# Kernel tuning notes

Hardware: AMD Instinct MI355X
Metric: run time of the kernel (lower is better)

## Reference

```python
import jax, jax.numpy as jnp
import numpy as np
import math

B, S, D, H, L, V = 16, 512, 1024, 16, 128, 32000
DH = D // H


def _posenc(s, d):
    pos = np.arange(s, dtype=np.float32)[:, None]
    div = np.exp(np.arange(0, d, 2, dtype=np.float32) * (-math.log(10000.0) / d))
    pe = np.zeros((s, d), dtype=np.float32)
    pe[:, 0::2] = np.sin(pos * div)
    pe[:, 1::2] = np.cos(pos * div)
    return jnp.asarray(pe)


def _ln(x, g, b):
    m = jnp.mean(x, axis=-1, keepdims=True)
    v = jnp.mean((x - m) ** 2, axis=-1, keepdims=True)
    return (x - m) / jnp.sqrt(v + 1e-5) * g + b


def setup_inputs():
    key = jax.random.key(0)
    ks = jax.random.split(key, 16)
    w = lambda k, *sh: 0.02 * jax.random.normal(k, sh, dtype=jnp.float32)
    return {
        'x': jax.random.randint(ks[0], (B, S), 0, V),
        'embed': w(ks[1], V, D),
        'Wq': w(ks[2], D, D), 'bq': jnp.zeros((D,), jnp.float32),
        'Wk': w(ks[3], D, D), 'bk': jnp.zeros((D,), jnp.float32),
        'Wv': w(ks[4], D, D), 'bv': jnp.zeros((D,), jnp.float32),
        'Wo': w(ks[5], D, D), 'bo': jnp.zeros((D,), jnp.float32),
        'g1': jnp.ones((D,), jnp.float32), 'be1': jnp.zeros((D,), jnp.float32),
        'W1': w(ks[6], D, D), 'bf1': jnp.zeros((D,), jnp.float32),
        'W2': w(ks[7], D, D), 'bf2': jnp.zeros((D,), jnp.float32),
        'g2': jnp.ones((D,), jnp.float32), 'be2': jnp.zeros((D,), jnp.float32),
        'g3': jnp.ones((D,), jnp.float32), 'be3': jnp.zeros((D,), jnp.float32),
        'Wmu': w(ks[8], D, L), 'bmu': jnp.zeros((L,), jnp.float32),
        'Wsig': w(ks[9], D, L), 'bsig': jnp.zeros((L,), jnp.float32),
        'eps': jax.random.normal(ks[10], (B, S, L), dtype=jnp.float32),
    }


def reference(x, embed, Wq, bq, Wk, bk, Wv, bv, Wo, bo, g1, be1, W1, bf1, W2, bf2,
              g2, be2, g3, be3, Wmu, bmu, Wsig, bsig, eps):
    h = embed[x] * jnp.asarray(D ** 0.5, jnp.float32)          # [B,S,D]
    h = h + _posenc(S, D)                                       # dropout = identity (eval)
    h = _ln(h, g1, be1)
    # attention (faithful to source: raw reshape head-split, scale = dh/2)
    Q = (h @ Wq + bq).reshape(B, H, S, DH)
    K = (h @ Wk + bk).reshape(B, H, S, DH)
    Vv = (h @ Wv + bv).reshape(B, H, S, DH)
    scores = jnp.einsum('bhqd,bhkd->bhqk', Q, K) / (DH / 2.0)
    attn = jax.nn.softmax(scores, axis=-1)
    ctx = jnp.einsum('bhqk,bhkd->bhqd', attn, Vv).reshape(B, S, D)
    ctx = ctx @ Wo + bo
    h = h + ctx
    h = _ln(h, g2, be2)
    f = jax.nn.leaky_relu(h @ W1 + bf1, 0.01) @ W2 + bf2
    h = f + f                                                    # source: x = ffn(x); x = x + drop2(x)
    h = _ln(h, g3, be3)
    mu = h @ Wmu + bmu
    sigma = jnp.exp(h @ Wsig + bsig)
    z = mu + sigma * eps
    return z
```

## Files before the change

### kernel.cpp

```cpp
#include <hip/hip_runtime.h>
#include <cstdint>


typedef __bf16 bf16;
typedef __bf16 bf16x8 __attribute__((ext_vector_type(8)));
typedef __bf16 bf16x4 __attribute__((ext_vector_type(4)));
typedef float f32x4 __attribute__((ext_vector_type(4)));

#define MFMA16(a, b, c) __builtin_amdgcn_mfma_f32_16x16x32_bf16((a), (b), (c), 0, 0, 0)

#if __has_builtin(__builtin_amdgcn_exp2f)
#define EXP2F(x) __builtin_amdgcn_exp2f(x)
#else
#define EXP2F(x) exp2f(x)
#endif

__device__ __forceinline__ void async16(const bf16* g, bf16* l) {
  __builtin_amdgcn_global_load_lds(
      (const __attribute__((address_space(1))) unsigned int*)g,
      (__attribute__((address_space(3))) unsigned int*)l, 16, 0, 0);
}

#define VMWAIT(N)                                        \
  do {                                                   \
    asm volatile("s_waitcnt vmcnt(" #N ")" ::: "memory"); \
    __builtin_amdgcn_sched_barrier(0);                   \
  } while (0)
#define BAR() __builtin_amdgcn_s_barrier()

__global__ __launch_bounds__(256) void zero_coefs_kernel(float* __restrict__ p) {
  p[blockIdx.x * 256 + threadIdx.x] = 0.f;
}

struct TP8 {
  const float* src[8];
  const float* gsrc[8];
  bf16* dst[8];
  int ncol[8];
};
__global__ __launch_bounds__(256) void transpose8_kernel(TP8 p) {
  const int z = blockIdx.z;
  const int N = p.ncol[z];
  const int tk = blockIdx.x * 64, tn = blockIdx.y * 64;
  if (tn >= N) return;
  const float* __restrict__ W = p.src[z];
  bf16* __restrict__ Wt = p.dst[z];
  __shared__ float tile[64][65];
  const int a = threadIdx.x >> 6, b = threadIdx.x & 63;
#pragma unroll
  for (int i = 0; i < 16; ++i) {
    int k = a + i * 4;
    tile[k][b] = W[(size_t)(tk + k) * N + tn + b];
  }
  __syncthreads();
  const float* gsc = p.gsrc[z];
  const float gv = gsc ? gsc[tk + b] : 1.0f;
#pragma unroll
  for (int i = 0; i < 16; ++i) {
    int n = a + i * 4;
    Wt[(size_t)(tn + n) * 1024 + tk + b] = (bf16)(tile[b][n] * gv);
  }
}

struct LC3 {
  const float* W[3];
  const float* g[3];
  const float* be[3];
  float* c1[3];
  float* c2[3];
  int N[3];
};
__global__ __launch_bounds__(256) void lncoef_kernel(LC3 p) {
  const int e = blockIdx.y;
  const int N = p.N[e];
  const int n0 = blockIdx.x * 64;
  if (n0 >= N) return;
  const int k0 = blockIdx.z * 64;
  const int w = threadIdx.x >> 6, lane = threadIdx.x & 63;
  const int n = n0 + lane;
  const float* __restrict__ W = p.W[e];
  const float* __restrict__ g = p.g[e];
  const float* __restrict__ be = p.be[e];
  float a1 = 0.f, a2 = 0.f;
#pragma unroll
  for (int i = 0; i < 16; ++i) {
    const int k = k0 + w * 16 + i;
    const float v = W[(size_t)k * N + n];
    a1 += g[k] * v;
    a2 += be[k] * v;
  }
  __shared__ float s1[4][64], s2[4][64];
  s1[w][lane] = a1;
  s2[w][lane] = a2;
  __syncthreads();
  if (w == 0) {
    a1 = s1[0][lane] + s1[1][lane] + s1[2][lane] + s1[3][lane];
    a2 = s2[0][lane] + s2[1][lane] + s2[2][lane] + s2[3][lane];
    atomicAdd(&p.c1[e][n], a1);
    atomicAdd(&p.c2[e][n], a2);
  }
}

__global__ __launch_bounds__(256) void embed_ln_kernel(const int* __restrict__ x,
                                                       const float* __restrict__ emb,
                                                       const float* __restrict__ g,
                                                       const float* __restrict__ be,
                                                       bf16* __restrict__ obf) {
  const int w = threadIdx.x >> 6, lane = threadIdx.x & 63;
  const int row = blockIdx.x * 4 + w;
  const int s = row & 511;
  const int t = x[row];
  const int c0 = lane * 16;
  const float* er = emb + (size_t)t * 1024 + c0;
  float o[16];
#pragma unroll
  for (int i = 0; i < 4; ++i) {
    const float4 e = *(const float4*)(er + i * 4);
    o[i * 4 + 0] = e.x; o[i * 4 + 1] = e.y; o[i * 4 + 2] = e.z; o[i * 4 + 3] = e.w;
  }
#pragma unroll
  for (int p = 0; p < 8; ++p) {
    const int cc = c0 + 2 * p;
    const float freq = __expf((float)cc * (-9.210340371976184f / 1024.0f));
    const float ang = (float)s * freq;
    o[2 * p] = o[2 * p] * 32.0f + __sinf(ang);
    o[2 * p + 1] = o[2 * p + 1] * 32.0f + __cosf(ang);
  }
  float sm = 0.f, q = 0.f;
#pragma unroll
  for (int j = 0; j < 16; ++j) { sm += o[j]; q += o[j] * o[j]; }
#pragma unroll
  for (int off = 1; off < 64; off <<= 1) {
    sm += __shfl_xor(sm, off);
    q += __shfl_xor(q, off);
  }
  const float mean = sm * (1.0f / 1024.0f);
  const float var = q * (1.0f / 1024.0f) - mean * mean;
  const float rstd = rsqrtf(var + 1e-5f);
  bf16 ob[16];
#pragma unroll
  for (int i = 0; i < 4; ++i) {
    const float4 gv = *(const float4*)(g + c0 + i * 4);
    const float4 bv = *(const float4*)(be + c0 + i * 4);
    const float gvv[4] = {gv.x, gv.y, gv.z, gv.w};
    const float bvv[4] = {bv.x, bv.y, bv.z, bv.w};
#pragma unroll
    for (int j = 0; j < 4; ++j)
      ob[i * 4 + j] = (bf16)((o[i * 4 + j] - mean) * rstd * gvv[j] + bvv[j]);
  }
  bf16* dst = obf + (size_t)row * 1024 + c0;
  *(uint4*)dst = *(const uint4*)&ob[0];
  *(uint4*)(dst + 8) = *(const uint4*)&ob[8];
}

__global__ __launch_bounds__(256) void rowstats_kernel(const bf16* __restrict__ in,
                                                       float* __restrict__ rs,
                                                       float* __restrict__ rm) {
  const int w = threadIdx.x >> 6, lane = threadIdx.x & 63;
  const int row = blockIdx.x * 4 + w;
  const int c0 = lane * 16;
  const bf16* src = in + (size_t)row * 1024 + c0;
  const bf16x8 v0 = *(const bf16x8*)src;
  const bf16x8 v1 = *(const bf16x8*)(src + 8);
  float s = 0.f, q = 0.f;
#pragma unroll
  for (int j = 0; j < 8; ++j) {
    const float a = (float)v0[j], b = (float)v1[j];
    s += a + b;
    q += a * a + b * b;
  }
#pragma unroll
  for (int off = 1; off < 64; off <<= 1) {
    s += __shfl_xor(s, off);
    q += __shfl_xor(q, off);
  }
  const float mean = s * (1.0f / 1024.0f);
  const float var = q * (1.0f / 1024.0f) - mean * mean;
  const float rstd = rsqrtf(var + 1e-5f);
  if (lane == 0) {
    rs[row] = rstd;
    rm[row] = -rstd * mean;
  }
}

__device__ __forceinline__ void ld_frags2(const bf16* sm, int rbase, int l15,
                                          int quad, bf16x8 out[2][2]) {
#pragma unroll
  for (int f = 0; f < 2; ++f) {
    const int row = rbase + f * 16 + l15;
    const int rx = row & 7;
#pragma unroll
    for (int h = 0; h < 2; ++h) {
      const int c = (h * 4 + quad) ^ rx;
      out[f][h] = *(const bf16x8*)(sm + (row * 8 + c) * 8);
    }
  }
}

template <int MQ, int NQ>
__device__ __forceinline__ void mma8(const bf16x8 aF[2][2], const bf16x8 bF[2][2],
                                     f32x4 acc[4][4]) {
  __builtin_amdgcn_s_setprio(1);
#pragma unroll
  for (int h = 0; h < 2; ++h)
#pragma unroll
    for (int m2 = 0; m2 < 2; ++m2)
#pragma unroll
      for (int n2 = 0; n2 < 2; ++n2)
        acc[MQ * 2 + m2][NQ * 2 + n2] =
            MFMA16(aF[m2][h], bF[n2][h], acc[MQ * 2 + m2][NQ * 2 + n2]);
  __builtin_amdgcn_s_setprio(0);
}

template <int MODE>
__global__ __launch_bounds__(512, 2) void gemm8_kernel(
    const bf16* __restrict__ A, const bf16* __restrict__ Bt,
    const float* __restrict__ b0f, const float* __restrict__ b1f,
    const float* __restrict__ b2f,
    bf16* __restrict__ o0, bf16* __restrict__ o1, bf16* __restrict__ o2,
    const bf16* __restrict__ residb,
    const float* __restrict__ rsP, const float* __restrict__ rmP,
    int M, int N, int K) {
  (void)M;
  __shared__ __attribute__((aligned(16))) bf16 Asm[2][128 * 64];
  __shared__ __attribute__((aligned(16))) bf16 Bsm[2][256 * 64];
  const int tid = threadIdx.x;
  const int wv = tid >> 6, lane = tid & 63;
  const int quad = lane >> 4, l15 = lane & 15;
  const int wm = wv & 1, wn = wv >> 1;
  const int m0 = blockIdx.x * 128, n0 = blockIdx.y * 256;

  f32x4 acc[4][4];
#pragma unroll
  for (int i = 0; i < 4; ++i)
#pragma unroll
    for (int j = 0; j < 4; ++j) acc[i][j] = {0.f, 0.f, 0.f, 0.f};

  size_t aoff[2], boff[2];
  int slds[2];
#pragma unroll
  for (int i = 0; i < 2; ++i) {
    const int s = tid + i * 512;
    const int r = s >> 3, c = (s & 7) ^ (r & 7);
    aoff[i] = (size_t)(m0 + r) * K + c * 8;
    boff[i] = (size_t)(n0 + r) * K + c * 8;
    slds[i] = s * 8;
  }
  auto stageA = [&](int buf, int t) {
#pragma unroll
    for (int i = 0; i < 2; ++i) async16(A + aoff[i] + t * 64, &Asm[buf][slds[i]]);
  };
  auto stageB = [&](int buf, int hh, int t) {
    const size_t ho = (size_t)hh * 128 * K;
    const int hl = hh * 8192;
#pragma unroll
    for (int i = 0; i < 2; ++i)
      async16(Bt + boff[i] + ho + t * 64, &Bsm[buf][hl + slds[i]]);
  };

  stageB(0, 0, 0); stageB(0, 1, 0); stageA(0, 0);
  stageB(1, 0, 1); stageB(1, 1, 1); stageA(1, 1);
  VMWAIT(6);
  BAR();

  bf16x8 aF[2][2], bF0[2][2], bF1[2][2];
  const int am0 = wm * 64, bn0 = wn * 64;

  auto phases = [&](int ne, int no, bool hn) {
    ld_frags2(&Asm[0][0], am0, l15, quad, aF);
    ld_frags2(&Bsm[0][0], bn0, l15, quad, bF0);
    BAR();
    mma8<0, 0>(aF, bF0, acc);
    BAR();
    ld_frags2(&Bsm[0][0], bn0 + 32, l15, quad, bF1);
    BAR();
    mma8<0, 1>(aF, bF1, acc);
    BAR();
    ld_frags2(&Asm[0][0], am0 + 32, l15, quad, aF);
    if (hn) stageB(0, 0, ne);
    BAR();
    mma8<1, 1>(aF, bF1, acc);
    BAR();
    if (hn) stageB(0, 1, ne);
    BAR();
    mma8<1, 0>(aF, bF0, acc);
    if (hn) { VMWAIT(4); } else { VMWAIT(0); }
    BAR();
    ld_frags2(&Asm[1][0], am0, l15, quad, aF);
    ld_frags2(&Bsm[1][0], bn0, l15, quad, bF0);
    if (hn) stageA(0, ne);
    BAR();
    mma8<0, 0>(aF, bF0, acc);
    BAR();
    ld_frags2(&Bsm[1][0], bn0 + 32, l15, quad, bF1);
    BAR();
    mma8<0, 1>(aF, bF1, acc);
    BAR();
    ld_frags2(&Asm[1][0], am0 + 32, l15, quad, aF);
    if (hn) stageB(1, 0, no);
    BAR();
    mma8<1, 1>(aF, bF1, acc);
    BAR();
    if (hn) { stageB(1, 1, no); stageA(1, no); }
    BAR();
    mma8<1, 0>(aF, bF0, acc);
    if (hn) { VMWAIT(6); }
    BAR();
  };

  const int nIter = K >> 7;
  for (int it = 0; it + 1 < nIter; ++it) phases(2 * it + 2, 2 * it + 3, true);
  phases(0, 0, false);

  const int part = (MODE == 6) ? ((int)blockIdx.y >> 2) : 0;
  bf16* ob = o0;
  const float* bp = b0f;
  if constexpr (MODE == 6) {
    ob = (part == 0) ? o0 : (part == 1 ? o1 : o2);
    bp = (part == 0) ? b0f : (part == 1 ? b1f : b2f);
  }
#pragma unroll
  for (int ni = 0; ni < 4; ++ni) {
    const int col = n0 + wn * 64 + ni * 16 + l15;
    const int cl = (MODE == 6) ? (col - part * 1024) : col;
    const float bv = bp[cl];
    float c1v = 0.f, c2v = 0.f;
    if constexpr (MODE == 4) { c1v = b1f[col]; c2v = b2f[col]; }
#pragma unroll
    for (int mi = 0; mi < 4; ++mi) {
#pragma unroll
      for (int r = 0; r < 4; ++r) {
        const int row = m0 + wm * 64 + mi * 16 + quad * 4 + r;
        const float a = acc[mi][ni][r];
        if constexpr (MODE == 1) {
          const size_t idx = (size_t)row * N + col;
          o0[idx] = (bf16)(a + bv + (float)residb[idx]);
        } else if constexpr (MODE == 4) {
          const float v = rsP[row] * a + rmP[row] * c1v + c2v + bv;
          o0[(size_t)row * N + col] = (bf16)(v > 0.f ? v : 0.01f * v);
        } else if constexpr (MODE == 3) {
          o0[(size_t)row * N + col] = (bf16)(2.0f * (a + bv));
        } else {
          ob[(size_t)row * 1024 + cl] = (bf16)(a + bv);
        }
      }
    }
  }
}

__global__ __launch_bounds__(256) void gemm_musig_z(
    const bf16* __restrict__ A, const bf16* __restrict__ Bt,
    const float* __restrict__ rsP, const float* __restrict__ rmP,
    const float* __restrict__ c1, const float* __restrict__ c2,
    const float* __restrict__ bmu, const float* __restrict__ bsig,
    const float* __restrict__ eps, float* __restrict__ z) {
  __shared__ __attribute__((aligned(16))) bf16 Asm[2][32 * 64];
  __shared__ __attribute__((aligned(16))) bf16 Bsm[2][256 * 64];
  const int tid = threadIdx.x;
  const int wv = tid >> 6, lane = tid & 63;
  const int quad = lane >> 4, l15 = lane & 15;
  const int m0 = blockIdx.x * 32;

  f32x4 acc[2][4];
#pragma unroll
  for (int i = 0; i < 2; ++i)
#pragma unroll
    for (int j = 0; j < 4; ++j) acc[i][j] = {0.f, 0.f, 0.f, 0.f};

  const bf16* Ag;
  int as_;
  {
    const int s = tid;
    const int r = s >> 3, c = (s & 7) ^ (r & 7);
    Ag = A + (size_t)(m0 + r) * 1024 + c * 8;
    as_ = s * 8;
  }
  const bf16* Bg[8];
  int bs_[8];
#pragma unroll
  for (int i = 0; i < 8; ++i) {
    const int s = tid + i * 256;
    const int r = s >> 3, c = (s & 7) ^ (r & 7);
    Bg[i] = Bt + (size_t)r * 1024 + c * 8;
    bs_[i] = s * 8;
  }

  async16(Ag, &Asm[0][as_]);
#pragma unroll
  for (int i = 0; i < 8; ++i) async16(Bg[i], &Bsm[0][bs_[i]]);
  __syncthreads();

  for (int k = 0; k < 16; ++k) {
    const int cur = k & 1, nxt = cur ^ 1;
    bf16x8 af[2][2], bfr[4][2];
#pragma unroll
    for (int mi = 0; mi < 2; ++mi) {
      const int row = mi * 16 + l15;
#pragma unroll
      for (int h = 0; h < 2; ++h) {
        const int pos = (h * 4 + quad) ^ (row & 7);
        af[mi][h] = *(const bf16x8*)(&Asm[cur][(row * 8 + pos) * 8]);
      }
    }
#pragma unroll
    for (int ni = 0; ni < 4; ++ni) {
      const int nr = (ni < 2 ? wv * 32 + ni * 16 : 128 + wv * 32 + (ni - 2) * 16) + l15;
#pragma unroll
      for (int h = 0; h < 2; ++h) {
        const int pos = (h * 4 + quad) ^ (nr & 7);
        bfr[ni][h] = *(const bf16x8*)(&Bsm[cur][(nr * 8 + pos) * 8]);
      }
    }
    if (k + 1 < 16) {
      const int ko = (k + 1) * 64;
      async16(Ag + ko, &Asm[nxt][as_]);
#pragma unroll
      for (int i = 0; i < 8; ++i) async16(Bg[i] + ko, &Bsm[nxt][bs_[i]]);
    }
#pragma unroll
    for (int h = 0; h < 2; ++h)
#pragma unroll
      for (int mi = 0; mi < 2; ++mi)
#pragma unroll
        for (int ni = 0; ni < 4; ++ni)
          acc[mi][ni] = MFMA16(af[mi][h], bfr[ni][h], acc[mi][ni]);
    __syncthreads();
  }

#pragma unroll
  for (int mi = 0; mi < 2; ++mi) {
#pragma unroll
    for (int r = 0; r < 4; ++r) {
      const int row = m0 + mi * 16 + quad * 4 + r;
      const float rs = rsP[row], rm = rmP[row];
#pragma unroll
      for (int cg = 0; cg < 2; ++cg) {
        const int cmu = wv * 32 + cg * 16 + l15;
        const int csg = 128 + cmu;
        const float mu = rs * acc[mi][cg][r] + rm * c1[cmu] + c2[cmu] + bmu[cmu];
        const float sg = rs * acc[mi][2 + cg][r] + rm * c1[csg] + c2[csg] + bsig[cmu];
        z[(size_t)row * 128 + cmu] = mu + __expf(sg) * eps[(size_t)row * 128 + cmu];
      }
    }
  }
}

__global__ __launch_bounds__(256) void vtrans_kernel(const bf16* __restrict__ Vb,
                                                     bf16* __restrict__ VtG) {
  __shared__ float t[64][65];
  const int bh = blockIdx.x, kt = blockIdx.y;
  const int tid = threadIdx.x;
  const bf16* src = Vb + (size_t)bh * 32768 + (size_t)kt * 4096;
#pragma unroll
  for (int i = 0; i < 2; ++i) {
    int s = i * 256 + tid;
    int r = s >> 3, c = (s & 7) * 8;
    bf16x8 v = *(const bf16x8*)(src + (size_t)s * 8);
#pragma unroll
    for (int j = 0; j < 8; ++j) t[r][c + j] = (float)v[j];
  }
  __syncthreads();
  bf16* dst = VtG + (size_t)bh * 32768 + kt * 64;
#pragma unroll
  for (int i = 0; i < 2; ++i) {
    int s = i * 256 + tid;
    int d = s >> 3, kc = (s & 7) * 8;
    bf16 tmp[8];
#pragma unroll
    for (int j = 0; j < 8; ++j) tmp[j] = (bf16)t[kc + j][d];
    *(uint4*)(dst + (size_t)d * 512 + kc) = *(const uint4*)tmp;
  }
}

__global__ __launch_bounds__(256) void attn_kernel(const bf16* __restrict__ Qg,
                                                   const bf16* __restrict__ Kg,
                                                   const bf16* __restrict__ Vt,
                                                   bf16* __restrict__ ctx) {
  __shared__ __attribute__((aligned(16))) bf16 Ksm[128 * 64];
  __shared__ __attribute__((aligned(16))) bf16 Vsm[64 * 128];
  __shared__ __attribute__((aligned(16))) bf16 Psm[4][16 * 128];
  const int tid = threadIdx.x;
  const int w = tid >> 6, lane = tid & 63;
  const int quad = lane >> 4, l15 = lane & 15;
  const int bh = blockIdx.x;
  const size_t base = (size_t)bh * 32768;
  const bf16* Vth = Vt + base;
  const int qbase = blockIdx.y * 128 + w * 32;
  const f32x4 fz = {0.f, 0.f, 0.f, 0.f};

  bf16x8 a[2][2];
#pragma unroll
  for (int qt = 0; qt < 2; ++qt)
#pragma unroll
    for (int hf = 0; hf < 2; ++hf) {
      bf16x8 tq = *(const bf16x8*)(Qg + base +
                   (size_t)(qbase + qt * 16 + l15) * 64 + hf * 32 + quad * 8);
#pragma unroll
      for (int e = 0; e < 8; ++e) tq[e] = (bf16)((float)tq[e] * 0.045111758f);
      a[qt][hf] = tq;
    }

  f32x4 o[2][4];
  float l_i[2][4];
#pragma unroll
  for (int qt = 0; qt < 2; ++qt)
#pragma unroll
    for (int i = 0; i < 4; ++i) { o[qt][i] = fz; l_i[qt][i] = 0.f; }

  for (int kv0 = 0; kv0 < 512; kv0 += 128) {
#pragma unroll
    for (int i = 0; i < 4; ++i) {
      int s = i * 256 + tid;
      int r = s >> 3, c = (s & 7) ^ (r & 7);
      async16(Kg + base + (size_t)(kv0 + r) * 64 + c * 8, &Ksm[s * 8]);
    }
#pragma unroll
    for (int i = 0; i < 4; ++i) {
      int s = i * 256 + tid;
      int d = s >> 4, cs = s & 15;
      int c = (cs & 8) | ((cs & 7) ^ (d & 7));
      async16(Vth + (size_t)d * 512 + kv0 + c * 8, &Vsm[s * 8]);
    }
    __syncthreads();

    f32x4 sc[2][8];
#pragma unroll
    for (int j = 0; j < 8; ++j) {
      const int n = j * 16 + l15;
      const bf16x8 k0 = *(const bf16x8*)(&Ksm[(n * 8 + (quad ^ (n & 7))) * 8]);
      const bf16x8 k1 = *(const bf16x8*)(&Ksm[(n * 8 + ((4 + quad) ^ (n & 7))) * 8]);
      sc[0][j] = MFMA16(a[0][0], k0, fz);
      sc[0][j] = MFMA16(a[0][1], k1, sc[0][j]);
      sc[1][j] = MFMA16(a[1][0], k0, fz);
      sc[1][j] = MFMA16(a[1][1], k1, sc[1][j]);
    }

    bf16* ps = &Psm[w][0];
#pragma unroll
    for (int qt = 0; qt < 2; ++qt) {
#pragma unroll
      for (int r = 0; r < 4; ++r) {
        const int prow = quad * 4 + r;
        float sum = 0.f;
#pragma unroll
        for (int j = 0; j < 8; ++j) {
          const float p = EXP2F(sc[qt][j][r]);
          sum += p;
          const int col = j * 16 + l15;
          const int cc = col >> 3;
          const int ccs = (cc & 8) | ((cc & 7) ^ (prow & 7));
          ps[prow * 128 + ccs * 8 + (col & 7)] = (bf16)p;
        }
        l_i[qt][r] += sum;
      }
#pragma unroll
      for (int c32 = 0; c32 < 4; ++c32) {
        const int pc = c32 * 4 + quad;
        const int pcs = (pc & 8) | ((pc & 7) ^ (l15 & 7));
        const bf16x8 pf = *(const bf16x8*)(ps + l15 * 128 + pcs * 8);
#pragma unroll
        for (int ni = 0; ni < 4; ++ni) {
          const int d = ni * 16 + l15;
          const int vcs = (pc & 8) | ((pc & 7) ^ (d & 7));
          const bf16x8 vf = *(const bf16x8*)(&Vsm[(d * 16 + vcs) * 8]);
          o[qt][ni] = MFMA16(pf, vf, o[qt][ni]);
        }
      }
    }
    __syncthreads();
  }

#pragma unroll
  for (int qt = 0; qt < 2; ++qt) {
#pragma unroll
    for (int r = 0; r < 4; ++r) {
      float l = l_i[qt][r];
      l += __shfl_xor(l, 1);
      l += __shfl_xor(l, 2);
      l += __shfl_xor(l, 4);
      l += __shfl_xor(l, 8);
      const float inv = 1.0f / l;
#pragma unroll
      for (int ni = 0; ni < 4; ++ni)
        ctx[base + (size_t)(qbase + qt * 16 + quad * 4 + r) * 64 + ni * 16 + l15]
            = (bf16)(o[qt][ni][r] * inv);
    }
  }
}

extern "C" void kernel_launch(void* const* d_in, const int* in_sizes, int n_in,
                              void* d_out, int out_size, void* d_ws, size_t ws_size,
                              hipStream_t stream) {
  (void)in_sizes; (void)n_in; (void)out_size; (void)ws_size;
  const int* x = (const int*)d_in[0];
  const float* emb = (const float*)d_in[1];
  const float* Wq = (const float*)d_in[2];
  const float* bq = (const float*)d_in[3];
  const float* Wk = (const float*)d_in[4];
  const float* bkb = (const float*)d_in[5];
  const float* Wv = (const float*)d_in[6];
  const float* bv = (const float*)d_in[7];
  const float* Wo = (const float*)d_in[8];
  const float* bo = (const float*)d_in[9];
  const float* g1 = (const float*)d_in[10];
  const float* be1 = (const float*)d_in[11];
  const float* W1 = (const float*)d_in[12];
  const float* bf1 = (const float*)d_in[13];
  const float* W2 = (const float*)d_in[14];
  const float* bf2 = (const float*)d_in[15];
  const float* g2 = (const float*)d_in[16];
  const float* be2 = (const float*)d_in[17];
  const float* g3 = (const float*)d_in[18];
  const float* be3 = (const float*)d_in[19];
  const float* Wmu = (const float*)d_in[20];
  const float* bmu = (const float*)d_in[21];
  const float* Wsig = (const float*)d_in[22];
  const float* bsig = (const float*)d_in[23];
  const float* eps = (const float*)d_in[24];
  float* z = (float*)d_out;

  const int M = 8192, D = 1024;
  char* ws = (char*)d_ws;
  size_t off = 0;
  auto alloc = [&](size_t b) {
    char* p = ws + off;
    off += (b + 255) & ~(size_t)255;
    return p;
  };
  bf16* wqkvT = (bf16*)alloc((size_t)3072 * 1024 * 2);
  bf16* woT = (bf16*)alloc((size_t)1024 * 1024 * 2);
  bf16* w1T = (bf16*)alloc((size_t)1024 * 1024 * 2);
  bf16* w2T = (bf16*)alloc((size_t)1024 * 1024 * 2);
  bf16* wmsT = (bf16*)alloc((size_t)256 * 1024 * 2);
  bf16* hb = (bf16*)alloc((size_t)M * D * 2);
  bf16* Qb = (bf16*)alloc((size_t)M * D * 2);
  bf16* Kb = (bf16*)alloc((size_t)M * D * 2);
  bf16* Vb = (bf16*)alloc((size_t)M * D * 2);
  bf16* VtG = (bf16*)alloc((size_t)M * D * 2);
  bf16* Cb = (bf16*)alloc((size_t)M * D * 2);
  bf16* h2b = (bf16*)alloc((size_t)M * D * 2);
  bf16* hidb = (bf16*)alloc((size_t)M * D * 2);
  bf16* h4b = (bf16*)alloc((size_t)M * D * 2);
  float* rs2 = (float*)alloc((size_t)M * 4);
  float* rm2 = (float*)alloc((size_t)M * 4);
  float* rs3 = (float*)alloc((size_t)M * 4);
  float* rm3 = (float*)alloc((size_t)M * 4);
  float* coefs = (float*)alloc((size_t)2560 * 4);
  float* c1w1 = coefs;
  float* c2w1 = coefs + 1024;
  float* c1ms = coefs + 2048;
  float* c2ms = coefs + 2304;

  dim3 b256(256);
  dim3 b512(512);

  zero_coefs_kernel<<<10, b256, 0, stream>>>(coefs);

  TP8 tp;
  for (int i = 0; i < 8; ++i) tp.gsrc[i] = nullptr;
  tp.src[0] = Wq;   tp.dst[0] = wqkvT;                        tp.ncol[0] = 1024;
  tp.src[1] = Wk;   tp.dst[1] = wqkvT + (size_t)1024 * 1024;  tp.ncol[1] = 1024;
  tp.src[2] = Wv;   tp.dst[2] = wqkvT + (size_t)2048 * 1024;  tp.ncol[2] = 1024;
  tp.src[3] = Wo;   tp.dst[3] = woT;                          tp.ncol[3] = 1024;
  tp.src[4] = W1;   tp.dst[4] = w1T;   tp.ncol[4] = 1024;     tp.gsrc[4] = g2;
  tp.src[5] = W2;   tp.dst[5] = w2T;                          tp.ncol[5] = 1024;
  tp.src[6] = Wmu;  tp.dst[6] = wmsT;  tp.ncol[6] = 128;      tp.gsrc[6] = g3;
  tp.src[7] = Wsig; tp.dst[7] = wmsT + (size_t)128 * 1024;    tp.ncol[7] = 128;
  tp.gsrc[7] = g3;
  transpose8_kernel<<<dim3(16, 16, 8), b256, 0, stream>>>(tp);

  LC3 lc;
  lc.W[0] = W1;   lc.g[0] = g2; lc.be[0] = be2; lc.c1[0] = c1w1;       lc.c2[0] = c2w1;       lc.N[0] = 1024;
  lc.W[1] = Wmu;  lc.g[1] = g3; lc.be[1] = be3; lc.c1[1] = c1ms;       lc.c2[1] = c2ms;       lc.N[1] = 128;
  lc.W[2] = Wsig; lc.g[2] = g3; lc.be[2] = be3; lc.c1[2] = c1ms + 128; lc.c2[2] = c2ms + 128; lc.N[2] = 128;
  lncoef_kernel<<<dim3(16, 3, 16), b256, 0, stream>>>(lc);

  embed_ln_kernel<<<2048, b256, 0, stream>>>(x, emb, g1, be1, hb);

  gemm8_kernel<6><<<dim3(64, 12), b512, 0, stream>>>(hb, wqkvT, bq, bkb, bv,
                                                     Qb, Kb, Vb, nullptr,
                                                     nullptr, nullptr, M, 3072, D);
  vtrans_kernel<<<dim3(256, 8), b256, 0, stream>>>(Vb, VtG);
  attn_kernel<<<dim3(256, 4), b256, 0, stream>>>(Qb, Kb, VtG, Cb);

  gemm8_kernel<1><<<dim3(64, 4), b512, 0, stream>>>(Cb, woT, bo, nullptr, nullptr,
                                                    h2b, nullptr, nullptr, hb,
                                                    nullptr, nullptr, M, D, D);
  rowstats_kernel<<<2048, b256, 0, stream>>>(h2b, rs2, rm2);
  gemm8_kernel<4><<<dim3(64, 4), b512, 0, stream>>>(h2b, w1T, bf1, c1w1, c2w1,
                                                    hidb, nullptr, nullptr, nullptr,
                                                    rs2, rm2, M, D, D);
  gemm8_kernel<3><<<dim3(64, 4), b512, 0, stream>>>(hidb, w2T, bf2, nullptr, nullptr,
                                                    h4b, nullptr, nullptr, nullptr,
                                                    nullptr, nullptr, M, D, D);
  rowstats_kernel<<<2048, b256, 0, stream>>>(h4b, rs3, rm3);
  gemm_musig_z<<<dim3(256), b256, 0, stream>>>(h4b, wmsT, rs3, rm3, c1ms, c2ms,
                                               bmu, bsig, eps, z);
}
```

Measured before the change: 431.6 us.

## Fuse LayerNorm row statistics into GEMM epilogues and LN coefficients into transpose

The two rowstats kernels are removed. Instead, the Wo and W2 GEMM epilogues accumulate per-row sum and sum-of-squares of their fp32 outputs using shuffles and atomics, and the consumers compute mean and rstd from those sums. The lncoef kernel is folded into the weight-transpose kernel, which reuses its shared-memory tile to build the gamma/beta projection coefficients. This removes three launches and two full re-reads of the activations. In exchange it adds global atomics per row segment and a larger zeroing pass, and the statistics now come from unrounded fp32 values instead of the bf16-stored outputs.

```diff
diff --git a/kernel.cpp b/kernel.cpp
--- a/kernel.cpp
+++ b/kernel.cpp
@@ -35,7 +35,10 @@
 struct TP8 {
   const float* src[8];
   const float* gsrc[8];
+  const float* besrc[8];
   bf16* dst[8];
+  float* c1dst[8];
+  float* c2dst[8];
   int ncol[8];
 };
 __global__ __launch_bounds__(256) void transpose8_kernel(TP8 p) {
@@ -46,6 +49,7 @@
   const float* __restrict__ W = p.src[z];
   bf16* __restrict__ Wt = p.dst[z];
   __shared__ float tile[64][65];
+  __shared__ float s1[4][64], s2[4][64];
   const int a = threadIdx.x >> 6, b = threadIdx.x & 63;
 #pragma unroll
   for (int i = 0; i < 16; ++i) {
@@ -60,44 +64,24 @@
     int n = a + i * 4;
     Wt[(size_t)(tn + n) * 1024 + tk + b] = (bf16)(tile[b][n] * gv);
   }
-}
-
-struct LC3 {
-  const float* W[3];
-  const float* g[3];
-  const float* be[3];
-  float* c1[3];
-  float* c2[3];
-  int N[3];
-};
-__global__ __launch_bounds__(256) void lncoef_kernel(LC3 p) {
-  const int e = blockIdx.y;
-  const int N = p.N[e];
-  const int n0 = blockIdx.x * 64;
-  if (n0 >= N) return;
-  const int k0 = blockIdx.z * 64;
-  const int w = threadIdx.x >> 6, lane = threadIdx.x & 63;
-  const int n = n0 + lane;
-  const float* __restrict__ W = p.W[e];
-  const float* __restrict__ g = p.g[e];
-  const float* __restrict__ be = p.be[e];
-  float a1 = 0.f, a2 = 0.f;
-#pragma unroll
-  for (int i = 0; i < 16; ++i) {
-    const int k = k0 + w * 16 + i;
-    const float v = W[(size_t)k * N + n];
-    a1 += g[k] * v;
-    a2 += be[k] * v;
-  }
-  __shared__ float s1[4][64], s2[4][64];
-  s1[w][lane] = a1;
-  s2[w][lane] = a2;
-  __syncthreads();
-  if (w == 0) {
-    a1 = s1[0][lane] + s1[1][lane] + s1[2][lane] + s1[3][lane];
-    a2 = s2[0][lane] + s2[1][lane] + s2[2][lane] + s2[3][lane];
-    atomicAdd(&p.c1[e][n], a1);
-    atomicAdd(&p.c2[e][n], a2);
+  if (p.c1dst[z]) {
+    const float* __restrict__ g = p.gsrc[z];
+    const float* __restrict__ be = p.besrc[z];
+    float a1 = 0.f, a2 = 0.f;
+#pragma unroll
+    for (int i = 0; i < 16; ++i) {
+      const int kk = a * 16 + i;
+      const float v = tile[kk][b];
+      a1 += g[tk + kk] * v;
+      a2 += be[tk + kk] * v;
+    }
+    s1[a][b] = a1;
+    s2[a][b] = a2;
+    __syncthreads();
+    if (a == 0) {
+      atomicAdd(&p.c1dst[z][tn + b], s1[0][b] + s1[1][b] + s1[2][b] + s1[3][b]);
+      atomicAdd(&p.c2dst[z][tn + b], s2[0][b] + s2[1][b] + s2[2][b] + s2[3][b]);
+    }
   }
 }
 
@@ -153,36 +137,6 @@
   *(uint4*)(dst + 8) = *(const uint4*)&ob[8];
 }
 
-__global__ __launch_bounds__(256) void rowstats_kernel(const bf16* __restrict__ in,
-                                                       float* __restrict__ rs,
-                                                       float* __restrict__ rm) {
-  const int w = threadIdx.x >> 6, lane = threadIdx.x & 63;
-  const int row = blockIdx.x * 4 + w;
-  const int c0 = lane * 16;
-  const bf16* src = in + (size_t)row * 1024 + c0;
-  const bf16x8 v0 = *(const bf16x8*)src;
-  const bf16x8 v1 = *(const bf16x8*)(src + 8);
-  float s = 0.f, q = 0.f;
-#pragma unroll
-  for (int j = 0; j < 8; ++j) {
-    const float a = (float)v0[j], b = (float)v1[j];
-    s += a + b;
-    q += a * a + b * b;
-  }
-#pragma unroll
-  for (int off = 1; off < 64; off <<= 1) {
-    s += __shfl_xor(s, off);
-    q += __shfl_xor(q, off);
-  }
-  const float mean = s * (1.0f / 1024.0f);
-  const float var = q * (1.0f / 1024.0f) - mean * mean;
-  const float rstd = rsqrtf(var + 1e-5f);
-  if (lane == 0) {
-    rs[row] = rstd;
-    rm[row] = -rstd * mean;
-  }
-}
-
 __device__ __forceinline__ void ld_frags2(const bf16* sm, int rbase, int l15,
                                           int quad, bf16x8 out[2][2]) {
 #pragma unroll
@@ -219,7 +173,8 @@
     const float* __restrict__ b2f,
     bf16* __restrict__ o0, bf16* __restrict__ o1, bf16* __restrict__ o2,
     const bf16* __restrict__ residb,
-    const float* __restrict__ rsP, const float* __restrict__ rmP,
+    const float* __restrict__ sumIn, const float* __restrict__ sqIn,
+    float* __restrict__ sumOut, float* __restrict__ sqOut,
     int M, int N, int K) {
   (void)M;
   __shared__ __attribute__((aligned(16))) bf16 Asm[2][128 * 64];
@@ -319,29 +274,61 @@
     ob = (part == 0) ? o0 : (part == 1 ? o1 : o2);
     bp = (part == 0) ? b0f : (part == 1 ? b1f : b2f);
   }
+
+  float bvv[4], c1v[4], c2v[4];
+  int cls[4];
 #pragma unroll
   for (int ni = 0; ni < 4; ++ni) {
     const int col = n0 + wn * 64 + ni * 16 + l15;
     const int cl = (MODE == 6) ? (col - part * 1024) : col;
-    const float bv = bp[cl];
-    float c1v = 0.f, c2v = 0.f;
-    if constexpr (MODE == 4) { c1v = b1f[col]; c2v = b2f[col]; }
-#pragma unroll
-    for (int mi = 0; mi < 4; ++mi) {
-#pragma unroll
-      for (int r = 0; r < 4; ++r) {
-        const int row = m0 + wm * 64 + mi * 16 + quad * 4 + r;
+    cls[ni] = cl;
+    bvv[ni] = bp[cl];
+    if constexpr (MODE == 4) { c1v[ni] = b1f[col]; c2v[ni] = b2f[col]; }
+    else { c1v[ni] = 0.f; c2v[ni] = 0.f; }
+  }
+
+#pragma unroll
+  for (int mi = 0; mi < 4; ++mi) {
+#pragma unroll
+    for (int r = 0; r < 4; ++r) {
+      const int row = m0 + wm * 64 + mi * 16 + quad * 4 + r;
+      float rstd = 0.f, rmean = 0.f;
+      if constexpr (MODE == 4) {
+        const float s = sumIn[row], q = sqIn[row];
+        const float mean = s * (1.0f / 1024.0f);
+        const float var = q * (1.0f / 1024.0f) - mean * mean;
+        rstd = rsqrtf(var + 1e-5f);
+        rmean = -rstd * mean;
+      }
+      float ps = 0.f, pq = 0.f;
+#pragma unroll
+      for (int ni = 0; ni < 4; ++ni) {
+        const int col = n0 + wn * 64 + ni * 16 + l15;
         const float a = acc[mi][ni][r];
         if constexpr (MODE == 1) {
           const size_t idx = (size_t)row * N + col;
-          o0[idx] = (bf16)(a + bv + (float)residb[idx]);
+          const float v = a + bvv[ni] + (float)residb[idx];
+          o0[idx] = (bf16)v;
+          ps += v; pq += v * v;
         } else if constexpr (MODE == 4) {
-          const float v = rsP[row] * a + rmP[row] * c1v + c2v + bv;
+          const float v = rstd * a + rmean * c1v[ni] + c2v[ni] + bvv[ni];
           o0[(size_t)row * N + col] = (bf16)(v > 0.f ? v : 0.01f * v);
         } else if constexpr (MODE == 3) {
-          o0[(size_t)row * N + col] = (bf16)(2.0f * (a + bv));
+          const float v = 2.0f * (a + bvv[ni]);
+          o0[(size_t)row * N + col] = (bf16)v;
+          ps += v; pq += v * v;
         } else {
-          ob[(size_t)row * 1024 + cl] = (bf16)(a + bv);
+          ob[(size_t)row * 1024 + cls[ni]] = (bf16)(a + bvv[ni]);
+        }
+      }
+      if constexpr (MODE == 1 || MODE == 3) {
+        ps += __shfl_xor(ps, 1); pq += __shfl_xor(pq, 1);
+        ps += __shfl_xor(ps, 2); pq += __shfl_xor(pq, 2);
+        ps += __shfl_xor(ps, 4); pq += __shfl_xor(pq, 4);
+        ps += __shfl_xor(ps, 8); pq += __shfl_xor(pq, 8);
+        if (l15 == 0) {
+          atomicAdd(&sumOut[row], ps);
+          atomicAdd(&sqOut[row], pq);
         }
       }
     }
@@ -350,7 +337,7 @@
 
 __global__ __launch_bounds__(256) void gemm_musig_z(
     const bf16* __restrict__ A, const bf16* __restrict__ Bt,
-    const float* __restrict__ rsP, const float* __restrict__ rmP,
+    const float* __restrict__ sumP, const float* __restrict__ sqP,
     const float* __restrict__ c1, const float* __restrict__ c2,
     const float* __restrict__ bmu, const float* __restrict__ bsig,
     const float* __restrict__ eps, float* __restrict__ z) {
@@ -432,7 +419,11 @@
 #pragma unroll
     for (int r = 0; r < 4; ++r) {
       const int row = m0 + mi * 16 + quad * 4 + r;
-      const float rs = rsP[row], rm = rmP[row];
+      const float s = sumP[row], q = sqP[row];
+      const float mean = s * (1.0f / 1024.0f);
+      const float var = q * (1.0f / 1024.0f) - mean * mean;
+      const float rs = rsqrtf(var + 1e-5f);
+      const float rm = -rs * mean;
 #pragma unroll
       for (int cg = 0; cg < 2; ++cg) {
         const int cmu = wv * 32 + cg * 16 + l15;
@@ -641,59 +632,60 @@
   bf16* h2b = (bf16*)alloc((size_t)M * D * 2);
   bf16* hidb = (bf16*)alloc((size_t)M * D * 2);
   bf16* h4b = (bf16*)alloc((size_t)M * D * 2);
-  float* rs2 = (float*)alloc((size_t)M * 4);
-  float* rm2 = (float*)alloc((size_t)M * 4);
-  float* rs3 = (float*)alloc((size_t)M * 4);
-  float* rm3 = (float*)alloc((size_t)M * 4);
-  float* coefs = (float*)alloc((size_t)2560 * 4);
+  float* coefs = (float*)alloc((size_t)35328 * 4);
   float* c1w1 = coefs;
   float* c2w1 = coefs + 1024;
   float* c1ms = coefs + 2048;
   float* c2ms = coefs + 2304;
+  float* sum2 = coefs + 2560;
+  float* sq2 = coefs + 10752;
+  float* sum3 = coefs + 18944;
+  float* sq3 = coefs + 27136;
 
   dim3 b256(256);
   dim3 b512(512);
 
-  zero_coefs_kernel<<<10, b256, 0, stream>>>(coefs);
+  zero_coefs_kernel<<<138, b256, 0, stream>>>(coefs);
 
   TP8 tp;
-  for (int i = 0; i < 8; ++i) tp.gsrc[i] = nullptr;
+  for (int i = 0; i < 8; ++i) {
+    tp.gsrc[i] = nullptr; tp.besrc[i] = nullptr;
+    tp.c1dst[i] = nullptr; tp.c2dst[i] = nullptr;
+  }
   tp.src[0] = Wq;   tp.dst[0] = wqkvT;                        tp.ncol[0] = 1024;
   tp.src[1] = Wk;   tp.dst[1] = wqkvT + (size_t)1024 * 1024;  tp.ncol[1] = 1024;
   tp.src[2] = Wv;   tp.dst[2] = wqkvT + (size_t)2048 * 1024;  tp.ncol[2] = 1024;
   tp.src[3] = Wo;   tp.dst[3] = woT;                          tp.ncol[3] = 1024;
-  tp.src[4] = W1;   tp.dst[4] = w1T;   tp.ncol[4] = 1024;     tp.gsrc[4] = g2;
+  tp.src[4] = W1;   tp.dst[4] = w1T;   tp.ncol[4] = 1024;
+  tp.gsrc[4] = g2;  tp.besrc[4] = be2; tp.c1dst[4] = c1w1;    tp.c2dst[4] = c2w1;
   tp.src[5] = W2;   tp.dst[5] = w2T;                          tp.ncol[5] = 1024;
-  tp.src[6] = Wmu;  tp.dst[6] = wmsT;  tp.ncol[6] = 128;      tp.gsrc[6] = g3;
+  tp.src[6] = Wmu;  tp.dst[6] = wmsT;  tp.ncol[6] = 128;
+  tp.gsrc[6] = g3;  tp.besrc[6] = be3; tp.c1dst[6] = c1ms;    tp.c2dst[6] = c2ms;
   tp.src[7] = Wsig; tp.dst[7] = wmsT + (size_t)128 * 1024;    tp.ncol[7] = 128;
-  tp.gsrc[7] = g3;
+  tp.gsrc[7] = g3;  tp.besrc[7] = be3; tp.c1dst[7] = c1ms + 128; tp.c2dst[7] = c2ms + 128;
   transpose8_kernel<<<dim3(16, 16, 8), b256, 0, stream>>>(tp);
-
-  LC3 lc;
-  lc.W[0] = W1;   lc.g[0] = g2; lc.be[0] = be2; lc.c1[0] = c1w1;       lc.c2[0] = c2w1;       lc.N[0] = 1024;
-  lc.W[1] = Wmu;  lc.g[1] = g3; lc.be[1] = be3; lc.c1[1] = c1ms;       lc.c2[1] = c2ms;       lc.N[1] = 128;
-  lc.W[2] = Wsig; lc.g[2] = g3; lc.be[2] = be3; lc.c1[2] = c1ms + 128; lc.c2[2] = c2ms + 128; lc.N[2] = 128;
-  lncoef_kernel<<<dim3(16, 3, 16), b256, 0, stream>>>(lc);
 
   embed_ln_kernel<<<2048, b256, 0, stream>>>(x, emb, g1, be1, hb);
 
   gemm8_kernel<6><<<dim3(64, 12), b512, 0, stream>>>(hb, wqkvT, bq, bkb, bv,
                                                      Qb, Kb, Vb, nullptr,
-                                                     nullptr, nullptr, M, 3072, D);
+                                                     nullptr, nullptr, nullptr,
+                                                     nullptr, M, 3072, D);
   vtrans_kernel<<<dim3(256, 8), b256, 0, stream>>>(Vb, VtG);
   attn_kernel<<<dim3(256, 4), b256, 0, stream>>>(Qb, Kb, VtG, Cb);
 
   gemm8_kernel<1><<<dim3(64, 4), b512, 0, stream>>>(Cb, woT, bo, nullptr, nullptr,
                                                     h2b, nullptr, nullptr, hb,
-                                                    nullptr, nullptr, M, D, D);
-  rowstats_kernel<<<2048, b256, 0, stream>>>(h2b, rs2, rm2);
+                                                    nullptr, nullptr, sum2, sq2,
+                                                    M, D, D);
   gemm8_kernel<4><<<dim3(64, 4), b512, 0, stream>>>(h2b, w1T, bf1, c1w1, c2w1,
                                                     hidb, nullptr, nullptr, nullptr,
-                                                    rs2, rm2, M, D, D);
+                                                    sum2, sq2, nullptr, nullptr,
+                                                    M, D, D);
   gemm8_kernel<3><<<dim3(64, 4), b512, 0, stream>>>(hidb, w2T, bf2, nullptr, nullptr,
                                                     h4b, nullptr, nullptr, nullptr,
-                                                    nullptr, nullptr, M, D, D);
-  rowstats_kernel<<<2048, b256, 0, stream>>>(h4b, rs3, rm3);
-  gemm_musig_z<<<dim3(256), b256, 0, stream>>>(h4b, wmsT, rs3, rm3, c1ms, c2ms,
+                                                    nullptr, nullptr, sum3, sq3,
+                                                    M, D, D);
+  gemm_musig_z<<<dim3(256), b256, 0, stream>>>(h4b, wmsT, sum3, sq3, c1ms, c2ms,
                                                bmu, bsig, eps, z);
 }
```

Result: no change. 428.0 us (-0.8%).
